# Optimization experiments

Measured on AMD Instinct MI355X. Metric: run time of the kernel, lower is better.

Reference implementation:

```python
import jax, jax.numpy as jnp
import numpy as np

N_NODES = 100000


def gcn_layer(x, edge_index, W, b, num_nodes):
    # GCNConv (PyG): h = x @ W; add self-loops; symmetric deg^-1/2 norm; scatter-add; + bias
    h = x @ W  # [N, out]
    loops = jnp.arange(num_nodes, dtype=edge_index.dtype)
    src = jnp.concatenate([edge_index[0], loops])
    dst = jnp.concatenate([edge_index[1], loops])
    deg = jax.ops.segment_sum(jnp.ones(src.shape[0], dtype=h.dtype), dst,
                              num_segments=num_nodes)  # includes self-loop, so deg >= 1
    dis = jax.lax.rsqrt(deg)  # deg^-1/2
    norm = dis[src] * dis[dst]  # [E+N]
    msg = h[src] * norm[:, None]  # gather + scale
    out = jax.ops.segment_sum(msg, dst, num_segments=num_nodes)  # scatter-add
    return out + b


def setup_inputs() -> dict:
    key = jax.random.key(0)
    k1, k2, k3, k4 = jax.random.split(key, 4)
    num_feature, hidden, num_label = 512, 16, 40
    n_edges = 3200000
    x = jax.random.normal(k1, (N_NODES, num_feature), dtype=jnp.float32)
    edge_index = jax.random.randint(k2, (2, n_edges), 0, N_NODES, dtype=jnp.int64)
    # Glorot-style init for weights
    W1 = jax.random.normal(k3, (num_feature, hidden), dtype=jnp.float32) / np.sqrt(num_feature)
    b1 = jnp.zeros((hidden,), dtype=jnp.float32)
    W2 = jax.random.normal(k4, (hidden, num_label), dtype=jnp.float32) / np.sqrt(hidden)
    b2 = jnp.zeros((num_label,), dtype=jnp.float32)
    return {"x": x, "edge_index": edge_index, "W1": W1, "b1": b1, "W2": W2, "b2": b2}


def reference(x, edge_index, W1, b1, W2, b2):
    h = gcn_layer(x, edge_index, W1, b1, N_NODES)
    h = jax.nn.relu(h)
    # dropout is identity in eval mode
    h = gcn_layer(h, edge_index, W2, b2, N_NODES)
    return jax.nn.log_softmax(h, axis=1)
```

## Files before the change

### kernel.cpp

```cpp
#include <hip/hip_runtime.h>
#include <math.h>

#define N_NODES 100000
#define N_EDGES 3200000
#define F_IN    512
#define H1      16
#define H2      40

#define NB      391
#define BSH     8
#define BMASK   255
#define B1      512
#define EPB     6250

__global__ void detect_idx_kernel(const int* __restrict__ ei, int* __restrict__ flag)
{
    if (threadIdx.x == 0 && blockIdx.x == 0) {
        int all_zero = 1;
        for (int i = 0; i < 64; ++i)
            if (ei[2 * i + 1] != 0) { all_zero = 0; break; }
        *flag = all_zero;
    }
}

__device__ __forceinline__ int edge_src(const void* ei, int e, int is64)
{
    return is64 ? (int)((const long long*)ei)[e] : ((const int*)ei)[e];
}
__device__ __forceinline__ int edge_dst(const void* ei, int e, int is64)
{
    return is64 ? (int)((const long long*)ei)[N_EDGES + e]
                : ((const int*)ei)[N_EDGES + e];
}

__global__ __launch_bounds__(256) void hist_kernel(
    const void* __restrict__ ei, const int* __restrict__ flag,
    int* __restrict__ cntoff)
{
    __shared__ int h[NB];
    for (int i = threadIdx.x; i < NB; i += 256) h[i] = 0;
    __syncthreads();
    const int is64 = *flag;
    const int e0 = blockIdx.x * EPB;
    for (int i = threadIdx.x; i < EPB; i += 256) {
        int e = e0 + i;
        if (e < N_EDGES) atomicAdd(&h[edge_dst(ei, e, is64) >> BSH], 1);
    }
    __syncthreads();
    for (int i = threadIdx.x; i < NB; i += 256)
        cntoff[blockIdx.x * NB + i] = h[i];
}

__global__ __launch_bounds__(256) void scanblk_kernel(
    int* __restrict__ cntoff, int* __restrict__ bstart)
{
    const int lane   = threadIdx.x & 63;
    const int bucket = blockIdx.x * 4 + (threadIdx.x >> 6);
    if (bucket >= NB) return;
    int run = 0;
    #pragma unroll
    for (int c = 0; c < B1 / 64; ++c) {
        const int i = c * 64 + lane;
        const int v = cntoff[i * NB + bucket];
        int s = v;
        #pragma unroll
        for (int off = 1; off < 64; off <<= 1) {
            int t = __shfl_up(s, off, 64);
            if (lane >= off) s += t;
        }
        cntoff[i * NB + bucket] = run + (s - v);
        run += __shfl(s, 63, 64);
    }
    if (lane == 0) bstart[bucket] = run;
}

__global__ __launch_bounds__(512) void scanb_kernel(int* __restrict__ bstart)
{
    __shared__ int s[512];
    const int t = threadIdx.x;
    const int v = (t < NB) ? bstart[t] : 0;
    s[t] = v;
    __syncthreads();
    for (int off = 1; off < 512; off <<= 1) {
        int tv = (t >= off) ? s[t - off] : 0;
        __syncthreads();
        s[t] += tv;
        __syncthreads();
    }
    if (t < NB) bstart[t] = s[t] - v;
    if (t == NB - 1) bstart[NB] = s[t];
}

__global__ __launch_bounds__(256) void scatter_bucket_kernel(
    const void* __restrict__ ei, const int* __restrict__ flag,
    const int* __restrict__ cntoff, const int* __restrict__ bstart,
    int* __restrict__ packed)
{
    __shared__ int cur[NB];
    for (int i = threadIdx.x; i < NB; i += 256)
        cur[i] = cntoff[blockIdx.x * NB + i] + bstart[i];
    __syncthreads();
    const int is64 = *flag;
    const int e0 = blockIdx.x * EPB;
    for (int i = threadIdx.x; i < EPB; i += 256) {
        int e = e0 + i;
        if (e >= N_EDGES) break;
        const int s = edge_src(ei, e, is64);
        const int d = edge_dst(ei, e, is64);
        const int b = d >> BSH;
        const int pos = atomicAdd(&cur[b], 1);
        packed[pos] = (s << BSH) | (d & BMASK);
    }
}

__global__ __launch_bounds__(512) void bucket_csr_kernel(
    const int* __restrict__ packed, const int* __restrict__ bstart,
    int* __restrict__ deg, int* __restrict__ row_end, int* __restrict__ csr)
{
    __shared__ int hist[256];
    __shared__ int off[256];
    const int b    = blockIdx.x;
    const int tid  = threadIdx.x;
    const int base = bstart[b];
    const int m    = bstart[b + 1] - base;

    if (tid < 256) hist[tid] = 0;
    __syncthreads();
    for (int i = tid; i < m; i += 512)
        atomicAdd(&hist[packed[base + i] & BMASK], 1);
    __syncthreads();

    int v = 0;
    if (tid < 256) { v = hist[tid]; off[tid] = v; }
    __syncthreads();
    for (int o = 1; o < 256; o <<= 1) {
        int t2 = 0;
        if (tid < 256 && tid >= o) t2 = off[tid - o];
        __syncthreads();
        if (tid < 256) off[tid] += t2;
        __syncthreads();
    }
    if (tid < 256) {
        const int g = (b << BSH) + tid;
        if (g < N_NODES) { deg[g] = v; row_end[g] = base + off[tid]; }
        off[tid] -= v;
    }
    __syncthreads();
    for (int i = tid; i < m; i += 512) {
        const int p = packed[base + i];
        const int pos = atomicAdd(&off[p & BMASK], 1);
        csr[base + pos] = p >> BSH;
    }
}

__global__ __launch_bounds__(64) void gemm1_kernel(
    const float* __restrict__ x, const float* __restrict__ W1,
    const int* __restrict__ deg, float* __restrict__ hs1,
    float* __restrict__ dis, int n)
{
    const int r = blockIdx.x * 64 + threadIdx.x;
    if (r >= n) return;

    const float4* xr = (const float4*)(x + (size_t)r * F_IN);
    float acc[H1];
    #pragma unroll
    for (int j = 0; j < H1; ++j) acc[j] = 0.f;

    #pragma unroll 4
    for (int k4 = 0; k4 < F_IN / 4; ++k4) {
        const float4 xv = xr[k4];
        const float* wk = W1 + k4 * 4 * H1;
        #pragma unroll
        for (int j = 0; j < H1; ++j)
            acc[j] += xv.x * wk[j] + xv.y * wk[H1 + j]
                    + xv.z * wk[2 * H1 + j] + xv.w * wk[3 * H1 + j];
    }

    const float dv = rsqrtf((float)deg[r] + 1.0f);
    dis[r] = dv;
    float4* o = (float4*)(hs1 + (size_t)r * H1);
    #pragma unroll
    for (int q = 0; q < 4; ++q) {
        float4 v;
        v.x = acc[4 * q + 0] * dv;
        v.y = acc[4 * q + 1] * dv;
        v.z = acc[4 * q + 2] * dv;
        v.w = acc[4 * q + 3] * dv;
        o[q] = v;
    }
}

template <int FUSE_L1>
__global__ __launch_bounds__(256) void pull16_kernel(
    const int* __restrict__ row_end, const int* __restrict__ csr,
    const float* __restrict__ rows, const float* __restrict__ dis,
    const float* __restrict__ b1, float* __restrict__ out, int n)
{
    int t = blockIdx.x * 256 + threadIdx.x;
    int g = t >> 2;
    int q = t & 3;
    if (g >= n) return;
    int beg = (g == 0) ? 0 : row_end[g - 1];
    int end = row_end[g];
    float4 acc = make_float4(0.f, 0.f, 0.f, 0.f);
    for (int i = beg; i < end; ++i) {
        int s = csr[i];
        float4 v = ((const float4*)(rows + (size_t)s * H1))[q];
        acc.x += v.x; acc.y += v.y; acc.z += v.z; acc.w += v.w;
    }
    if (FUSE_L1) {
        const float dv = dis[g];
        float4 h = ((const float4*)(rows + (size_t)g * H1))[q];
        float4 bq = ((const float4*)b1)[q];
        acc.x = dv * fmaxf(dv * (acc.x + h.x) + bq.x, 0.f);
        acc.y = dv * fmaxf(dv * (acc.y + h.y) + bq.y, 0.f);
        acc.z = dv * fmaxf(dv * (acc.z + h.z) + bq.z, 0.f);
        acc.w = dv * fmaxf(dv * (acc.w + h.w) + bq.w, 0.f);
    }
    ((float4*)(out + (size_t)g * H1))[q] = acc;
}

__global__ __launch_bounds__(256) void epi_kernel(
    const float* __restrict__ agg2, const float* __restrict__ c,
    const float* __restrict__ W2, const float* __restrict__ b2,
    const float* __restrict__ dis, float* __restrict__ out, int n)
{
    __shared__ float w[H1 * H2];
    for (int t = threadIdx.x; t < H1 * H2; t += 256) w[t] = W2[t];
    __syncthreads();

    const int row  = blockIdx.x * 4 + (threadIdx.x >> 6);
    if (row >= n) return;
    const int lane = threadIdx.x & 63;

    float tv = 0.f;
    if (lane < H1)
        tv = agg2[(size_t)row * H1 + lane] + c[(size_t)row * H1 + lane];

    const float dv = dis[row];
    float val = -INFINITY;
    if (lane < H2) {
        float s = 0.f;
        #pragma unroll
        for (int k = 0; k < H1; ++k) {
            float tk = __shfl(tv, k, 64);
            s += tk * w[k * H2 + lane];
        }
        val = dv * s + b2[lane];
    }
    float m = val;
    #pragma unroll
    for (int off = 32; off > 0; off >>= 1) m = fmaxf(m, __shfl_xor(m, off, 64));
    float ex = (lane < H2) ? __expf(val - m) : 0.f;
    #pragma unroll
    for (int off = 32; off > 0; off >>= 1) ex += __shfl_xor(ex, off, 64);
    if (lane < H2) out[(size_t)row * H2 + lane] = val - m - logf(ex);
}

extern "C" void kernel_launch(void* const* d_in, const int* in_sizes, int n_in,
                              void* d_out, int out_size, void* d_ws, size_t ws_size,
                              hipStream_t stream)
{
    const float* x   = (const float*)d_in[0];
    const void*  ei  = d_in[1];
    const float* W1  = (const float*)d_in[2];
    const float* b1  = (const float*)d_in[3];
    const float* W2  = (const float*)d_in[4];
    const float* b2  = (const float*)d_in[5];
    float*       out = (float*)d_out;

    int*   base    = (int*)d_ws;
    int*   flag    = base;
    int*   deg     = base + 16;
    int*   row_end = deg + N_NODES;
    int*   bstart  = row_end + N_NODES;
    int*   cntoff  = bstart + 512;
    float* dis     = (float*)(cntoff + B1 * NB);
    int*   csr     = (int*)(dis + N_NODES);
    int*   packed  = csr + N_EDGES;
    float* hs1     = (float*)packed;
    float* c       = hs1 + (size_t)N_NODES * H1;
    float* agg2    = hs1;

    detect_idx_kernel<<<1, 64, 0, stream>>>((const int*)ei, flag);

    hist_kernel<<<B1, 256, 0, stream>>>(ei, flag, cntoff);
    scanblk_kernel<<<(NB + 3) / 4, 256, 0, stream>>>(cntoff, bstart);
    scanb_kernel<<<1, 512, 0, stream>>>(bstart);
    scatter_bucket_kernel<<<B1, 256, 0, stream>>>(ei, flag, cntoff, bstart, packed);
    bucket_csr_kernel<<<NB, 512, 0, stream>>>(packed, bstart, deg, row_end, csr);

    gemm1_kernel<<<(N_NODES + 63) / 64, 64, 0, stream>>>(x, W1, deg, hs1, dis, N_NODES);

    const int PB = (N_NODES * 4 + 255) / 256;
    pull16_kernel<1><<<PB, 256, 0, stream>>>(row_end, csr, hs1, dis, b1, c, N_NODES);
    pull16_kernel<0><<<PB, 256, 0, stream>>>(row_end, csr, c, dis, b1, agg2, N_NODES);

    epi_kernel<<<(N_NODES + 3) / 4, 256, 0, stream>>>(agg2, c, W2, b2, dis, out, N_NODES);
}
```

Baseline: 298.0 us.

## Split first-layer GEMM K dimension across two blocks and add combine kernel

```diff
diff --git a/kernel.cpp b/kernel.cpp
--- a/kernel.cpp
+++ b/kernel.cpp
@@ -153,41 +153,58 @@
     }
 }
 
-__global__ __launch_bounds__(64) void gemm1_kernel(
+__global__ __launch_bounds__(256) void gemm1_kernel(
     const float* __restrict__ x, const float* __restrict__ W1,
-    const int* __restrict__ deg, float* __restrict__ hs1,
-    float* __restrict__ dis, int n)
-{
-    const int r = blockIdx.x * 64 + threadIdx.x;
+    float* __restrict__ partial, int n)
+{
+    const int rb = blockIdx.x >> 1;
+    const int h  = blockIdx.x & 1;
+    const int r  = rb * 256 + threadIdx.x;
     if (r >= n) return;
 
-    const float4* xr = (const float4*)(x + (size_t)r * F_IN);
+    const float4* xr = (const float4*)(x + (size_t)r * F_IN) + h * 64;
+    const float*  Wb = W1 + h * (F_IN / 2) * H1;
+
     float acc[H1];
     #pragma unroll
     for (int j = 0; j < H1; ++j) acc[j] = 0.f;
 
-    #pragma unroll 4
-    for (int k4 = 0; k4 < F_IN / 4; ++k4) {
+    #pragma unroll 8
+    for (int k4 = 0; k4 < 64; ++k4) {
         const float4 xv = xr[k4];
-        const float* wk = W1 + k4 * 4 * H1;
+        const float* wk = Wb + k4 * 4 * H1;
         #pragma unroll
         for (int j = 0; j < H1; ++j)
             acc[j] += xv.x * wk[j] + xv.y * wk[H1 + j]
                     + xv.z * wk[2 * H1 + j] + xv.w * wk[3 * H1 + j];
     }
 
-    const float dv = rsqrtf((float)deg[r] + 1.0f);
-    dis[r] = dv;
-    float4* o = (float4*)(hs1 + (size_t)r * H1);
+    float4* o = (float4*)(partial + (size_t)h * N_NODES * H1 + (size_t)r * H1);
     #pragma unroll
     for (int q = 0; q < 4; ++q) {
         float4 v;
-        v.x = acc[4 * q + 0] * dv;
-        v.y = acc[4 * q + 1] * dv;
-        v.z = acc[4 * q + 2] * dv;
-        v.w = acc[4 * q + 3] * dv;
+        v.x = acc[4 * q + 0]; v.y = acc[4 * q + 1];
+        v.z = acc[4 * q + 2]; v.w = acc[4 * q + 3];
         o[q] = v;
     }
+}
+
+__global__ __launch_bounds__(256) void combine_kernel(
+    float* __restrict__ partial, const int* __restrict__ deg,
+    float* __restrict__ dis, int n)
+{
+    int t = blockIdx.x * 256 + threadIdx.x;
+    int g = t >> 2;
+    int q = t & 3;
+    if (g >= n) return;
+    float4 a = ((const float4*)(partial + (size_t)g * H1))[q];
+    float4 b = ((const float4*)(partial + (size_t)N_NODES * H1 + (size_t)g * H1))[q];
+    const float dv = rsqrtf((float)deg[g] + 1.0f);
+    if (q == 0) dis[g] = dv;
+    float4 o;
+    o.x = (a.x + b.x) * dv; o.y = (a.y + b.y) * dv;
+    o.z = (a.z + b.z) * dv; o.w = (a.w + b.w) * dv;
+    ((float4*)(partial + (size_t)g * H1))[q] = o;
 }
 
 template <int FUSE_L1>
@@ -277,8 +294,10 @@
     int*   cntoff  = bstart + 512;
     float* dis     = (float*)(cntoff + B1 * NB);
     int*   csr     = (int*)(dis + N_NODES);
-    int*   packed  = csr + N_EDGES;
-    float* hs1     = (float*)packed;
+    int*   REGION  = csr + N_EDGES;
+    int*   packed  = REGION;
+    float* partial = (float*)REGION;
+    float* hs1     = partial;
     float* c       = hs1 + (size_t)N_NODES * H1;
     float* agg2    = hs1;
 
@@ -290,9 +309,12 @@
     scatter_bucket_kernel<<<B1, 256, 0, stream>>>(ei, flag, cntoff, bstart, packed);
     bucket_csr_kernel<<<NB, 512, 0, stream>>>(packed, bstart, deg, row_end, csr);
 
-    gemm1_kernel<<<(N_NODES + 63) / 64, 64, 0, stream>>>(x, W1, deg, hs1, dis, N_NODES);
+    const int RB = (N_NODES + 255) / 256;
+    gemm1_kernel<<<2 * RB, 256, 0, stream>>>(x, W1, partial, N_NODES);
 
     const int PB = (N_NODES * 4 + 255) / 256;
+    combine_kernel<<<PB, 256, 0, stream>>>(partial, deg, dis, N_NODES);
+
     pull16_kernel<1><<<PB, 256, 0, stream>>>(row_end, csr, hs1, dis, b1, c, N_NODES);
     pull16_kernel<0><<<PB, 256, 0, stream>>>(row_end, csr, c, dis, b1, agg2, N_NODES);
 
```

New measurement: 304.7 us. 1.02x slower.

## Stage x tiles into LDS with async double-buffered global_load_lds in GEMM1

Applied to the files above, without the earlier changes.

```diff
diff --git a/kernel.cpp b/kernel.cpp
--- a/kernel.cpp
+++ b/kernel.cpp
@@ -12,6 +12,10 @@
 #define BMASK   255
 #define B1      512
 #define EPB     6250
+
+#define GROWS   256
+#define KT      32
+#define NKT     (F_IN / KT)
 
 __global__ void detect_idx_kernel(const int* __restrict__ ei, int* __restrict__ flag)
 {
@@ -153,40 +157,82 @@
     }
 }
 
-__global__ __launch_bounds__(64) void gemm1_kernel(
+__global__ __launch_bounds__(256) void gemm1_kernel(
     const float* __restrict__ x, const float* __restrict__ W1,
     const int* __restrict__ deg, float* __restrict__ hs1,
     float* __restrict__ dis, int n)
 {
-    const int r = blockIdx.x * 64 + threadIdx.x;
-    if (r >= n) return;
-
-    const float4* xr = (const float4*)(x + (size_t)r * F_IN);
+    __shared__ __attribute__((aligned(16))) float lds[2][GROWS * KT];
+
+    const int tid  = threadIdx.x;
+    const int wave = tid >> 6;
+    const int lane = tid & 63;
+    const int r0   = blockIdx.x * GROWS;
+
+    const int lrow  = lane >> 3;
+    const int lslot = lane & 7;
+    const int lchunk = lslot ^ lrow;
+
+    auto issue = [&](int kt, int buf) {
+        #pragma unroll
+        for (int ii = 0; ii < 8; ++ii) {
+            int row_g = r0 + wave * 64 + ii * 8 + lrow;
+            if (row_g > n - 1) row_g = n - 1;
+            const float* g = x + (size_t)row_g * F_IN + kt * KT + lchunk * 4;
+            float* l = &lds[buf][(wave * 8 + ii) * 256];
+            __builtin_amdgcn_global_load_lds(
+                (const __attribute__((address_space(1))) void*)g,
+                (__attribute__((address_space(3))) void*)l,
+                16, 0, 0);
+        }
+    };
+
     float acc[H1];
     #pragma unroll
     for (int j = 0; j < H1; ++j) acc[j] = 0.f;
 
-    #pragma unroll 4
-    for (int k4 = 0; k4 < F_IN / 4; ++k4) {
-        const float4 xv = xr[k4];
-        const float* wk = W1 + k4 * 4 * H1;
-        #pragma unroll
-        for (int j = 0; j < H1; ++j)
-            acc[j] += xv.x * wk[j] + xv.y * wk[H1 + j]
-                    + xv.z * wk[2 * H1 + j] + xv.w * wk[3 * H1 + j];
-    }
-
-    const float dv = rsqrtf((float)deg[r] + 1.0f);
-    dis[r] = dv;
-    float4* o = (float4*)(hs1 + (size_t)r * H1);
-    #pragma unroll
-    for (int q = 0; q < 4; ++q) {
-        float4 v;
-        v.x = acc[4 * q + 0] * dv;
-        v.y = acc[4 * q + 1] * dv;
-        v.z = acc[4 * q + 2] * dv;
-        v.w = acc[4 * q + 3] * dv;
-        o[q] = v;
+    issue(0, 0);
+
+    for (int kt = 0; kt < NKT; ++kt) {
+        const int buf = kt & 1;
+        if (kt + 1 < NKT) {
+            issue(kt + 1, buf ^ 1);
+            asm volatile("s_waitcnt vmcnt(8)" ::: "memory");
+        } else {
+            asm volatile("s_waitcnt vmcnt(0)" ::: "memory");
+        }
+        __builtin_amdgcn_s_barrier();
+        __builtin_amdgcn_sched_barrier(0);
+        #pragma unroll
+        for (int c = 0; c < 8; ++c) {
+            const float4 xv =
+                *(const float4*)&lds[buf][tid * KT + ((c ^ (tid & 7)) << 2)];
+            const float* wk = W1 + (kt * KT + c * 4) * H1;
+            #pragma unroll
+            for (int j = 0; j < H1; ++j) {
+                acc[j] = fmaf(xv.x, wk[j],          acc[j]);
+                acc[j] = fmaf(xv.y, wk[H1 + j],     acc[j]);
+                acc[j] = fmaf(xv.z, wk[2 * H1 + j], acc[j]);
+                acc[j] = fmaf(xv.w, wk[3 * H1 + j], acc[j]);
+            }
+        }
+        __builtin_amdgcn_s_barrier();
+    }
+
+    const int r = r0 + tid;
+    if (r < n) {
+        const float dv = rsqrtf((float)deg[r] + 1.0f);
+        dis[r] = dv;
+        float4* o = (float4*)(hs1 + (size_t)r * H1);
+        #pragma unroll
+        for (int q = 0; q < 4; ++q) {
+            float4 v;
+            v.x = acc[4 * q + 0] * dv;
+            v.y = acc[4 * q + 1] * dv;
+            v.z = acc[4 * q + 2] * dv;
+            v.w = acc[4 * q + 3] * dv;
+            o[q] = v;
+        }
     }
 }
 
@@ -277,8 +323,9 @@
     int*   cntoff  = bstart + 512;
     float* dis     = (float*)(cntoff + B1 * NB);
     int*   csr     = (int*)(dis + N_NODES);
-    int*   packed  = csr + N_EDGES;
-    float* hs1     = (float*)packed;
+    int*   REGION  = csr + N_EDGES;
+    int*   packed  = REGION;
+    float* hs1     = (float*)REGION;
     float* c       = hs1 + (size_t)N_NODES * H1;
     float* agg2    = hs1;
 
@@ -290,7 +337,8 @@
     scatter_bucket_kernel<<<B1, 256, 0, stream>>>(ei, flag, cntoff, bstart, packed);
     bucket_csr_kernel<<<NB, 512, 0, stream>>>(packed, bstart, deg, row_end, csr);
 
-    gemm1_kernel<<<(N_NODES + 63) / 64, 64, 0, stream>>>(x, W1, deg, hs1, dis, N_NODES);
+    gemm1_kernel<<<(N_NODES + GROWS - 1) / GROWS, 256, 0, stream>>>(
+        x, W1, deg, hs1, dis, N_NODES);
 
     const int PB = (N_NODES * 4 + 255) / 256;
     pull16_kernel<1><<<PB, 256, 0, stream>>>(row_end, csr, hs1, dis, b1, c, N_NODES);
```

New measurement: 298.0 us. About the same (-0.0%).

## Fuse CSR bucket build using global atomics and fixed-capacity buckets

Applied to the files above, without the earlier changes.

```diff
diff --git a/kernel.cpp b/kernel.cpp
--- a/kernel.cpp
+++ b/kernel.cpp
@@ -12,6 +12,7 @@
 #define BMASK   255
 #define B1      512
 #define EPB     6250
+#define CAP     9216
 
 __global__ void detect_idx_kernel(const int* __restrict__ ei, int* __restrict__ flag)
 {
@@ -33,11 +34,12 @@
                 : ((const int*)ei)[N_EDGES + e];
 }
 
-__global__ __launch_bounds__(256) void hist_kernel(
+__global__ __launch_bounds__(256) void scatter_atomic_kernel(
     const void* __restrict__ ei, const int* __restrict__ flag,
-    int* __restrict__ cntoff)
+    int* __restrict__ cnt, int* __restrict__ packed)
 {
     __shared__ int h[NB];
+    __shared__ int cur[NB];
     for (int i = threadIdx.x; i < NB; i += 256) h[i] = 0;
     __syncthreads();
     const int is64 = *flag;
@@ -47,87 +49,45 @@
         if (e < N_EDGES) atomicAdd(&h[edge_dst(ei, e, is64) >> BSH], 1);
     }
     __syncthreads();
-    for (int i = threadIdx.x; i < NB; i += 256)
-        cntoff[blockIdx.x * NB + i] = h[i];
-}
-
-__global__ __launch_bounds__(256) void scanblk_kernel(
-    int* __restrict__ cntoff, int* __restrict__ bstart)
-{
-    const int lane   = threadIdx.x & 63;
-    const int bucket = blockIdx.x * 4 + (threadIdx.x >> 6);
-    if (bucket >= NB) return;
-    int run = 0;
-    #pragma unroll
-    for (int c = 0; c < B1 / 64; ++c) {
-        const int i = c * 64 + lane;
-        const int v = cntoff[i * NB + bucket];
-        int s = v;
-        #pragma unroll
-        for (int off = 1; off < 64; off <<= 1) {
-            int t = __shfl_up(s, off, 64);
-            if (lane >= off) s += t;
-        }
-        cntoff[i * NB + bucket] = run + (s - v);
-        run += __shfl(s, 63, 64);
-    }
-    if (lane == 0) bstart[bucket] = run;
-}
-
-__global__ __launch_bounds__(512) void scanb_kernel(int* __restrict__ bstart)
-{
-    __shared__ int s[512];
-    const int t = threadIdx.x;
-    const int v = (t < NB) ? bstart[t] : 0;
-    s[t] = v;
-    __syncthreads();
-    for (int off = 1; off < 512; off <<= 1) {
-        int tv = (t >= off) ? s[t - off] : 0;
-        __syncthreads();
-        s[t] += tv;
-        __syncthreads();
-    }
-    if (t < NB) bstart[t] = s[t] - v;
-    if (t == NB - 1) bstart[NB] = s[t];
-}
-
-__global__ __launch_bounds__(256) void scatter_bucket_kernel(
-    const void* __restrict__ ei, const int* __restrict__ flag,
-    const int* __restrict__ cntoff, const int* __restrict__ bstart,
-    int* __restrict__ packed)
-{
-    __shared__ int cur[NB];
-    for (int i = threadIdx.x; i < NB; i += 256)
-        cur[i] = cntoff[blockIdx.x * NB + i] + bstart[i];
-    __syncthreads();
-    const int is64 = *flag;
-    const int e0 = blockIdx.x * EPB;
+    for (int i = threadIdx.x; i < NB; i += 256) {
+        int base = (h[i] > 0) ? atomicAdd(&cnt[i], h[i]) : 0;
+        cur[i] = i * CAP + base;
+    }
+    __syncthreads();
     for (int i = threadIdx.x; i < EPB; i += 256) {
         int e = e0 + i;
         if (e >= N_EDGES) break;
         const int s = edge_src(ei, e, is64);
         const int d = edge_dst(ei, e, is64);
-        const int b = d >> BSH;
-        const int pos = atomicAdd(&cur[b], 1);
+        const int pos = atomicAdd(&cur[d >> BSH], 1);
         packed[pos] = (s << BSH) | (d & BMASK);
     }
 }
 
 __global__ __launch_bounds__(512) void bucket_csr_kernel(
-    const int* __restrict__ packed, const int* __restrict__ bstart,
-    int* __restrict__ deg, int* __restrict__ row_end, int* __restrict__ csr)
+    const int* __restrict__ packed, const int* __restrict__ cnt,
+    int* __restrict__ deg, int* __restrict__ row_beg, int* __restrict__ csr)
 {
     __shared__ int hist[256];
     __shared__ int off[256];
-    const int b    = blockIdx.x;
-    const int tid  = threadIdx.x;
-    const int base = bstart[b];
-    const int m    = bstart[b + 1] - base;
-
+    __shared__ int sbase;
+    const int b   = blockIdx.x;
+    const int tid = threadIdx.x;
+
+    if (tid < 64) {
+        int s = 0;
+        for (int i = tid; i < b; i += 64) s += cnt[i];
+        #pragma unroll
+        for (int o = 32; o > 0; o >>= 1) s += __shfl_xor(s, o, 64);
+        if (tid == 0) sbase = s;
+    }
     if (tid < 256) hist[tid] = 0;
     __syncthreads();
+
+    const int base_in = b * CAP;
+    const int m       = cnt[b];
     for (int i = tid; i < m; i += 512)
-        atomicAdd(&hist[packed[base + i] & BMASK], 1);
+        atomicAdd(&hist[packed[base_in + i] & BMASK], 1);
     __syncthreads();
 
     int v = 0;
@@ -141,15 +101,16 @@
         __syncthreads();
     }
     if (tid < 256) {
+        const int excl = sbase + off[tid] - v;
         const int g = (b << BSH) + tid;
-        if (g < N_NODES) { deg[g] = v; row_end[g] = base + off[tid]; }
-        off[tid] -= v;
+        if (g < N_NODES) { deg[g] = v; row_beg[g] = excl; }
+        off[tid] = excl;
     }
     __syncthreads();
     for (int i = tid; i < m; i += 512) {
-        const int p = packed[base + i];
+        const int p = packed[base_in + i];
         const int pos = atomicAdd(&off[p & BMASK], 1);
-        csr[base + pos] = p >> BSH;
+        csr[pos] = p >> BSH;
     }
 }
 
@@ -192,22 +153,33 @@
 
 template <int FUSE_L1>
 __global__ __launch_bounds__(256) void pull16_kernel(
-    const int* __restrict__ row_end, const int* __restrict__ csr,
-    const float* __restrict__ rows, const float* __restrict__ dis,
-    const float* __restrict__ b1, float* __restrict__ out, int n)
+    const int* __restrict__ row_beg, const int* __restrict__ deg,
+    const int* __restrict__ csr, const float* __restrict__ rows,
+    const float* __restrict__ dis, const float* __restrict__ b1,
+    float* __restrict__ out, int n)
 {
     int t = blockIdx.x * 256 + threadIdx.x;
     int g = t >> 2;
     int q = t & 3;
     if (g >= n) return;
-    int beg = (g == 0) ? 0 : row_end[g - 1];
-    int end = row_end[g];
-    float4 acc = make_float4(0.f, 0.f, 0.f, 0.f);
-    for (int i = beg; i < end; ++i) {
-        int s = csr[i];
-        float4 v = ((const float4*)(rows + (size_t)s * H1))[q];
+    const int beg = row_beg[g];
+    const int end = beg + deg[g];
+    float4 acc  = make_float4(0.f, 0.f, 0.f, 0.f);
+    float4 acc2 = make_float4(0.f, 0.f, 0.f, 0.f);
+    int i = beg;
+    for (; i + 1 < end; i += 2) {
+        int s0 = csr[i];
+        int s1 = csr[i + 1];
+        float4 v0 = ((const float4*)(rows + (size_t)s0 * H1))[q];
+        float4 v1 = ((const float4*)(rows + (size_t)s1 * H1))[q];
+        acc.x  += v0.x; acc.y  += v0.y; acc.z  += v0.z; acc.w  += v0.w;
+        acc2.x += v1.x; acc2.y += v1.y; acc2.z += v1.z; acc2.w += v1.w;
+    }
+    if (i < end) {
+        float4 v = ((const float4*)(rows + (size_t)csr[i] * H1))[q];
         acc.x += v.x; acc.y += v.y; acc.z += v.z; acc.w += v.w;
     }
+    acc.x += acc2.x; acc.y += acc2.y; acc.z += acc2.z; acc.w += acc2.w;
     if (FUSE_L1) {
         const float dv = dis[g];
         float4 h = ((const float4*)(rows + (size_t)g * H1))[q];
@@ -272,29 +244,26 @@
     int*   base    = (int*)d_ws;
     int*   flag    = base;
     int*   deg     = base + 16;
-    int*   row_end = deg + N_NODES;
-    int*   bstart  = row_end + N_NODES;
-    int*   cntoff  = bstart + 512;
-    float* dis     = (float*)(cntoff + B1 * NB);
+    int*   row_beg = deg + N_NODES;
+    int*   cnt     = row_beg + N_NODES;
+    float* dis     = (float*)(cnt + 512);
     int*   csr     = (int*)(dis + N_NODES);
     int*   packed  = csr + N_EDGES;
     float* hs1     = (float*)packed;
     float* c       = hs1 + (size_t)N_NODES * H1;
     float* agg2    = hs1;
 
+    hipMemsetAsync(cnt, 0, 512 * sizeof(int), stream);
     detect_idx_kernel<<<1, 64, 0, stream>>>((const int*)ei, flag);
 
-    hist_kernel<<<B1, 256, 0, stream>>>(ei, flag, cntoff);
-    scanblk_kernel<<<(NB + 3) / 4, 256, 0, stream>>>(cntoff, bstart);
-    scanb_kernel<<<1, 512, 0, stream>>>(bstart);
-    scatter_bucket_kernel<<<B1, 256, 0, stream>>>(ei, flag, cntoff, bstart, packed);
-    bucket_csr_kernel<<<NB, 512, 0, stream>>>(packed, bstart, deg, row_end, csr);
+    scatter_atomic_kernel<<<B1, 256, 0, stream>>>(ei, flag, cnt, packed);
+    bucket_csr_kernel<<<NB, 512, 0, stream>>>(packed, cnt, deg, row_beg, csr);
 
     gemm1_kernel<<<(N_NODES + 63) / 64, 64, 0, stream>>>(x, W1, deg, hs1, dis, N_NODES);
 
     const int PB = (N_NODES * 4 + 255) / 256;
-    pull16_kernel<1><<<PB, 256, 0, stream>>>(row_end, csr, hs1, dis, b1, c, N_NODES);
-    pull16_kernel<0><<<PB, 256, 0, stream>>>(row_end, csr, c, dis, b1, agg2, N_NODES);
+    pull16_kernel<1><<<PB, 256, 0, stream>>>(row_beg, deg, csr, hs1, dis, b1, c, N_NODES);
+    pull16_kernel<0><<<PB, 256, 0, stream>>>(row_beg, deg, csr, c, dis, b1, agg2, N_NODES);
 
     epi_kernel<<<(N_NODES + 3) / 4, 256, 0, stream>>>(agg2, c, W2, b2, dis, out, N_NODES);
 }
```

Result: no change. 298.9 us (+0.3%).
